# Kernel optimization log

Hardware: AMD Instinct MI355X
Metric: run time of the kernel (lower is better)

The kernel has to match this reference:

```python
import jax, jax.numpy as jnp
import numpy as np

N, E, B = 100000, 800000, 64
IN, HC1, HC2, NC, SA = 256, 128, 32, 2, 350
NEG = 0.2  # GATv2Conv default negative_slope


def forward(s_x, s_edge_index, s_batch, s_root_n_id,
            Wq, bq, Wk, bk, Wv, bv,
            Wl1, bl1, Wr1, br1, att1, bias1,
            Wl2, bl2, Wr2, br2, att2, bias2,
            Wl3, bl3, Wr3, br3, att3, bias3,
            c1w, c1b, c2W, c2b, c3W, c3b,
            linW, linb, aW1, ab1, aW2, mW1, mb1, mW2, mb2):
    src, dst = s_edge_index[0], s_edge_index[1]
    x_info = s_x
    # --- SelfAttention over seq_len=1 (x.unsqueeze(1)) ---
    z = s_x[:, None, :]                                   # [N,1,IN]
    q = z @ Wq + bq; k = z @ Wk + bk; v = z @ Wv + bv      # [N,1,SA]
    scores = jnp.einsum('nqd,nkd->nqk', q, k) / jnp.sqrt(jnp.float32(SA))
    probs = jax.nn.softmax(scores, axis=-1)
    h = jnp.einsum('nqk,nkd->nqd', probs, v)[:, 0, :]      # [N,SA]

    def gatv2(x, Wl, bl, Wr, br, att, bias):
        # PyG GATv2Conv, heads=1, eval mode (dropout off)
        xl = x @ Wl + bl                                   # source transform [N,O]
        xr = x @ Wr + br                                   # target transform [N,O]
        e = jax.nn.leaky_relu(xl[src] + xr[dst], NEG)      # [E,O]
        s = e @ att                                        # [E]
        smax = jax.ops.segment_max(s, dst, num_segments=N)
        smax = jnp.where(jnp.isfinite(smax), smax, 0.0)
        ex = jnp.exp(s - smax[dst])
        den = jax.ops.segment_sum(ex, dst, num_segments=N)
        alpha = ex / jnp.maximum(den[dst], 1e-16)
        return jax.ops.segment_sum(alpha[:, None] * xl[src], dst, num_segments=N) + bias

    h = jax.nn.relu(gatv2(h, Wl1, bl1, Wr1, br1, att1, bias1))
    h = jax.nn.relu(gatv2(h, Wl2, bl2, Wr2, br2, att2, bias2))
    h = jax.nn.relu(gatv2(h, Wl3, bl3, Wr3, br3, att3, bias3))   # [N,HC2]

    # --- readout: root node feature ++ global mean pool ---
    cnt = jax.ops.segment_sum(jnp.ones((N,), h.dtype), s_batch, num_segments=B)
    pooled = jax.ops.segment_sum(h, s_batch, num_segments=B) / jnp.maximum(cnt, 1.0)[:, None]
    sx = jnp.concatenate([h[s_root_n_id], pooled], axis=-1)       # [B,2*HC2]

    # --- info branch on raw root features ---
    info = x_info[s_root_n_id]                                    # [B,IN]
    info = c1w[0] * info[:, :-2] + c1w[1] * info[:, 1:-1] + c1w[2] * info[:, 2:] + c1b  # Conv1d(1,1,3)
    t = info.T                                                    # [IN-2,B]
    t = jax.nn.relu(c2W @ t + c2b[:, None])                       # [HC1,B]
    t = jax.nn.relu(c3W @ t + c3b[:, None])                       # [HC1//2,B]
    t = t.T                                                       # [B,HC1//2]
    L = t.shape[1]
    t = jax.nn.relu(t.reshape(B, HC2, L // HC2).mean(-1))         # AdaptiveAvgPool1d(HC2)

    sx = jax.nn.relu(sx @ linW + linb)                            # [B,HC2]

    # --- semantic attention over the two views ---
    emb = jnp.stack([sx, t], axis=1)                              # [B,2,HC2]
    w = jnp.tanh(emb @ aW1 + ab1) @ aW2                           # [B,2,1]
    beta = jax.nn.softmax(w, axis=1)
    emb = (beta * emb).sum(1)                                     # [B,HC2]

    return jax.nn.softmax(jnp.tanh(emb @ mW1 + mb1) @ mW2 + mb2, axis=1)  # [B,NC]


def setup_inputs() -> dict:
    keys = iter(jax.random.split(jax.random.key(0), 64))
    def nrm(*shape):
        return jax.random.normal(next(keys), shape, dtype=jnp.float32) * 0.05
    inp = {}
    inp['s_x'] = jax.random.normal(next(keys), (N, IN), dtype=jnp.float32)
    inp['s_edge_index'] = jax.random.randint(next(keys), (2, E), 0, N)
    inp['s_batch'] = jnp.sort(jax.random.randint(next(keys), (N,), 0, B))
    inp['s_root_n_id'] = jax.random.randint(next(keys), (B,), 0, N)
    inp['Wq'] = nrm(IN, SA); inp['bq'] = nrm(SA)
    inp['Wk'] = nrm(IN, SA); inp['bk'] = nrm(SA)
    inp['Wv'] = nrm(IN, SA); inp['bv'] = nrm(SA)
    inp['Wl1'] = nrm(SA, HC1); inp['bl1'] = nrm(HC1)
    inp['Wr1'] = nrm(SA, HC1); inp['br1'] = nrm(HC1)
    inp['att1'] = nrm(HC1); inp['bias1'] = nrm(HC1)
    inp['Wl2'] = nrm(HC1, HC1 // 2); inp['bl2'] = nrm(HC1 // 2)
    inp['Wr2'] = nrm(HC1, HC1 // 2); inp['br2'] = nrm(HC1 // 2)
    inp['att2'] = nrm(HC1 // 2); inp['bias2'] = nrm(HC1 // 2)
    inp['Wl3'] = nrm(HC1 // 2, HC2); inp['bl3'] = nrm(HC2)
    inp['Wr3'] = nrm(HC1 // 2, HC2); inp['br3'] = nrm(HC2)
    inp['att3'] = nrm(HC2); inp['bias3'] = nrm(HC2)
    inp['c1w'] = nrm(3); inp['c1b'] = nrm(1)
    inp['c2W'] = nrm(HC1, IN - 2); inp['c2b'] = nrm(HC1)
    inp['c3W'] = nrm(HC1 // 2, HC1); inp['c3b'] = nrm(HC1 // 2)
    inp['linW'] = nrm(2 * HC2, HC2); inp['linb'] = nrm(HC2)
    inp['aW1'] = nrm(HC2, 16); inp['ab1'] = nrm(16); inp['aW2'] = nrm(16, 1)
    inp['mW1'] = nrm(HC2, 16); inp['mb1'] = nrm(16)
    inp['mW2'] = nrm(16, NC); inp['mb2'] = nrm(NC)
    return inp


def reference(s_x, s_edge_index, s_batch, s_root_n_id,
              Wq, bq, Wk, bk, Wv, bv,
              Wl1, bl1, Wr1, br1, att1, bias1,
              Wl2, bl2, Wr2, br2, att2, bias2,
              Wl3, bl3, Wr3, br3, att3, bias3,
              c1w, c1b, c2W, c2b, c3W, c3b,
              linW, linb, aW1, ab1, aW2, mW1, mb1, mW2, mb2):
    return forward(s_x, s_edge_index, s_batch, s_root_n_id,
                   Wq, bq, Wk, bk, Wv, bv,
                   Wl1, bl1, Wr1, br1, att1, bias1,
                   Wl2, bl2, Wr2, br2, att2, bias2,
                   Wl3, bl3, Wr3, br3, att3, bias3,
                   c1w, c1b, c2W, c2b, c3W, c3b,
                   linW, linb, aW1, ab1, aW2, mW1, mb1, mW2, mb2)
```

## Files before the change

### kernel.cpp

```cpp
#include <hip/hip_runtime.h>
#include <hip/hip_bf16.h>
#include <math.h>

typedef unsigned short ushort_t;
typedef __attribute__((ext_vector_type(8))) short bfrag;
typedef __attribute__((ext_vector_type(4))) float ffrag;

constexpr int N_NODES = 100000;
constexpr int N_EDGES = 800000;
constexpr int NB      = 64;
constexpr int IN_F    = 256;
constexpr int HC1C    = 128;
constexpr int HC2C    = 32;
constexpr int SA_D    = 350;
constexpr float NEG   = 0.2f;

constexpr int SCAN_NBLK = (N_NODES + 255) / 256;
constexpr int MB128     = (N_NODES + 127) / 128;

constexpr size_t OFF_WT1    = 0;
constexpr size_t OFF_WT2    = OFF_WT1 + 65536;
constexpr size_t OFF_WT3    = OFF_WT2 + 16384;
constexpr size_t OFF_BC1    = OFF_WT3 + 4096;
constexpr size_t OFF_BC2    = OFF_BC1 + 256;
constexpr size_t OFF_BC3    = OFF_BC2 + 128;
constexpr size_t OFF_XLR    = OFF_BC3 + 64;
constexpr size_t OFF_H      = OFF_XLR + (size_t)N_NODES * 256;
constexpr size_t OFF_DEG    = OFF_H + (size_t)N_NODES * 128;
constexpr size_t OFF_ROWPTR = OFF_DEG + N_NODES;
constexpr size_t OFF_CURSOR = OFF_ROWPTR + N_NODES + 1;
constexpr size_t OFF_BLKS   = OFF_CURSOR + N_NODES;
constexpr size_t OFF_BLKO   = OFF_BLKS + 512;
constexpr size_t OFF_CSRSRC = OFF_BLKO + 512;
constexpr size_t OFF_POOLED = OFF_CSRSRC + N_EDGES;
constexpr size_t OFF_CNT    = OFF_POOLED + NB * HC2C;
constexpr size_t OFF_SX     = OFF_CNT + NB;
constexpr size_t OFF_INFO   = OFF_SX + NB * HC2C;
constexpr size_t OFF_T1     = OFF_INFO + (size_t)NB * (IN_F - 2);
constexpr size_t OFF_T2     = OFF_T1 + (size_t)HC1C * NB;
constexpr size_t OFF_TT     = OFF_T2 + (size_t)NB * NB;
constexpr size_t WS_FLOATS  = OFF_TT + NB * HC2C;

__device__ __forceinline__ ushort_t f2bf(float f) {
  union { float f; unsigned int u; } a;
  a.f = f;
  unsigned int r = a.u + 0x7FFFu + ((a.u >> 16) & 1u);
  return (ushort_t)(r >> 16);
}
__device__ __forceinline__ float bf2f(ushort_t h) {
  union { unsigned int u; float f; } a;
  a.u = ((unsigned int)h) << 16;
  return a.f;
}
__device__ __forceinline__ float2 bfp(unsigned int u) {
  float2 r;
  r.x = __uint_as_float(u << 16);
  r.y = __uint_as_float(u & 0xFFFF0000u);
  return r;
}
__device__ __forceinline__ unsigned int pack2(float a, float b) {
  unsigned int ua = __float_as_uint(a);
  ua += 0x7FFFu + ((ua >> 16) & 1u);
  unsigned int ub = __float_as_uint(b);
  ub += 0x7FFFu + ((ub >> 16) & 1u);
  return __builtin_amdgcn_perm(ub, ua, 0x07060302u);
}

__global__ void k_wcomb(const float* __restrict__ Wv, const float* __restrict__ Wl1,
                        const float* __restrict__ Wr1, ushort_t* __restrict__ WT) {
  int t = blockIdx.x * blockDim.x + threadIdx.x;
  if (t >= 256 * 256) return;
  int n = t & 255;
  int k = t >> 8;
  const float* Wx = (n < 128) ? Wl1 : Wr1;
  int j = n & 127;
  float a = 0.f;
  for (int kk = 0; kk < SA_D; ++kk) a += Wv[k * SA_D + kk] * Wx[kk * 128 + j];
  WT[(size_t)n * 256 + k] = f2bf(a);
}

__global__ void k_bcomb(const float* __restrict__ bv, const float* __restrict__ Wl1,
                        const float* __restrict__ bl1, const float* __restrict__ Wr1,
                        const float* __restrict__ br1, float* __restrict__ bc) {
  int n = threadIdx.x;
  if (n >= 256) return;
  const float* Wx = (n < 128) ? Wl1 : Wr1;
  const float* bx = (n < 128) ? bl1 : br1;
  int j = n & 127;
  float a = bx[j];
  for (int kk = 0; kk < SA_D; ++kk) a += bv[kk] * Wx[kk * 128 + j];
  bc[n] = a;
}

template <int K, int C>
__global__ void k_wpack(const float* __restrict__ Wl, const float* __restrict__ bl,
                        const float* __restrict__ Wr, const float* __restrict__ br,
                        ushort_t* __restrict__ WT, float* __restrict__ bc) {
  constexpr int NN = 2 * C;
  int t = blockIdx.x * blockDim.x + threadIdx.x;
  if (t < NN) bc[t] = (t < C) ? bl[t] : br[t - C];
  if (t >= NN * K) return;
  int n = t % NN;
  int k = t / NN;
  float v = (n < C) ? Wl[k * C + n] : Wr[k * C + (n - C)];
  WT[(size_t)n * K + k] = f2bf(v);
}

__global__ void k_hist(const int* __restrict__ dst, int* __restrict__ deg) {
  int e = blockIdx.x * blockDim.x + threadIdx.x;
  if (e < N_EDGES) atomicAdd(deg + dst[e], 1);
}

__global__ void k_scan_local(const int* __restrict__ deg, int* __restrict__ row_ptr,
                             int* __restrict__ blk_sum) {
  __shared__ int sh[256];
  int t = threadIdx.x;
  int i = blockIdx.x * 256 + t;
  int v = (i < N_NODES) ? deg[i] : 0;
  sh[t] = v;
  __syncthreads();
  for (int off = 1; off < 256; off <<= 1) {
    int add = (t >= off) ? sh[t - off] : 0;
    __syncthreads();
    sh[t] += add;
    __syncthreads();
  }
  if (i < N_NODES) row_ptr[i] = sh[t] - v;
  if (t == 255) blk_sum[blockIdx.x] = sh[255];
}

__global__ void k_scan_blk(const int* __restrict__ blk_sum, int* __restrict__ blk_off) {
  __shared__ int sh[512];
  int t = threadIdx.x;
  int v = (t < SCAN_NBLK) ? blk_sum[t] : 0;
  sh[t] = v;
  __syncthreads();
  for (int off = 1; off < 512; off <<= 1) {
    int add = (t >= off) ? sh[t - off] : 0;
    __syncthreads();
    sh[t] += add;
    __syncthreads();
  }
  blk_off[t] = sh[t] - v;
}

__global__ void k_scan_add(int* __restrict__ row_ptr, const int* __restrict__ blk_off,
                           int* __restrict__ cursor) {
  int i = blockIdx.x * blockDim.x + threadIdx.x;
  if (i < N_NODES) {
    int v = row_ptr[i] + blk_off[i >> 8];
    row_ptr[i] = v;
    cursor[i] = v;
  }
  if (i == 0) row_ptr[N_NODES] = N_EDGES;
}

__global__ void k_fill(const int* __restrict__ src, const int* __restrict__ dst,
                       int* __restrict__ cursor, int* __restrict__ csr_src) {
  int e = blockIdx.x * blockDim.x + threadIdx.x;
  if (e >= N_EDGES) return;
  int pos = atomicAdd(cursor + dst[e], 1);
  csr_src[pos] = src[e];
}

template <int K, int NN, int BN, bool AF32>
__global__ __launch_bounds__(256) void k_gemm_bf16(const void* __restrict__ xin,
                                                   const ushort_t* __restrict__ WT,
                                                   const float* __restrict__ bc,
                                                   ushort_t* __restrict__ out, int M) {
  constexpr int BM    = 128;
  constexpr int BK    = 32;
  constexpr int LDA   = BK + 8;
  constexpr int RT    = 4;
  constexpr int CT    = BN / 32;
  constexpr int NSTEP = K / BK;
  constexpr int NBCH  = (BN * 4) / 256;
  __shared__ ushort_t As[2][BM * LDA];
  __shared__ ushort_t Bs[2][BN * LDA];
  const int tid  = threadIdx.x;
  const int wave = tid >> 6;
  const int wrow = wave >> 1;
  const int wcol = wave & 1;
  const int lane = tid & 63;
  const int quad = lane >> 4;
  const int l16  = lane & 15;
  const int m0   = blockIdx.x * BM;
  const int n0   = blockIdx.y * BN;

  const int arow = tid >> 1;
  const int aks  = (tid & 1) * 16;
  int gm = m0 + arow;
  if (gm >= M) gm = M - 1;

  float4 fA[4];
  uint4  uA[2];
  uint4  uB[NBCH];

  auto loadT = [&](int k0) {
    if (AF32) {
      const float4* sp = (const float4*)((const float*)xin + (size_t)gm * K + k0 + aks);
      fA[0] = sp[0]; fA[1] = sp[1]; fA[2] = sp[2]; fA[3] = sp[3];
    } else {
      const uint4* sp = (const uint4*)((const ushort_t*)xin + (size_t)gm * K + k0 + aks);
      uA[0] = sp[0]; uA[1] = sp[1];
    }
#pragma unroll
    for (int c = 0; c < NBCH; ++c) {
      int ch = tid + c * 256;
      int n  = ch >> 2;
      int ks = (ch & 3) * 8;
      uB[c] = *(const uint4*)(WT + (size_t)(n0 + n) * K + k0 + ks);
    }
  };
  auto storeT = [&](int buf) {
    if (AF32) {
      uint4 p0, p1;
      p0.x = pack2(fA[0].x, fA[0].y); p0.y = pack2(fA[0].z, fA[0].w);
      p0.z = pack2(fA[1].x, fA[1].y); p0.w = pack2(fA[1].z, fA[1].w);
      p1.x = pack2(fA[2].x, fA[2].y); p1.y = pack2(fA[2].z, fA[2].w);
      p1.z = pack2(fA[3].x, fA[3].y); p1.w = pack2(fA[3].z, fA[3].w);
      *(uint4*)&As[buf][arow * LDA + aks]     = p0;
      *(uint4*)&As[buf][arow * LDA + aks + 8] = p1;
    } else {
      *(uint4*)&As[buf][arow * LDA + aks]     = uA[0];
      *(uint4*)&As[buf][arow * LDA + aks + 8] = uA[1];
    }
#pragma unroll
    for (int c = 0; c < NBCH; ++c) {
      int ch = tid + c * 256;
      int n  = ch >> 2;
      int ks = (ch & 3) * 8;
      *(uint4*)&Bs[buf][n * LDA + ks] = uB[c];
    }
  };

  ffrag acc[RT][CT];
#pragma unroll
  for (int rt = 0; rt < RT; ++rt)
#pragma unroll
    for (int ct = 0; ct < CT; ++ct) acc[rt][ct] = ffrag{0.f, 0.f, 0.f, 0.f};

  loadT(0);
  storeT(0);
  __syncthreads();

  for (int i = 0; i < NSTEP; ++i) {
    const int cur = i & 1;
    if (i + 1 < NSTEP) loadT((i + 1) * BK);
    bfrag a[RT], b[CT];
#pragma unroll
    for (int rt = 0; rt < RT; ++rt)
      a[rt] = *(const bfrag*)&As[cur][(wrow * 64 + rt * 16 + l16) * LDA + quad * 8];
#pragma unroll
    for (int ct = 0; ct < CT; ++ct)
      b[ct] = *(const bfrag*)&Bs[cur][(wcol * (BN / 2) + ct * 16 + l16) * LDA + quad * 8];
#pragma unroll
    for (int ct = 0; ct < CT; ++ct)
#pragma unroll
      for (int rt = 0; rt < RT; ++rt)
        acc[rt][ct] = __builtin_amdgcn_mfma_f32_16x16x32_bf16(a[rt], b[ct], acc[rt][ct], 0, 0, 0);
    if (i + 1 < NSTEP) storeT(1 - cur);
    __syncthreads();
  }

#pragma unroll
  for (int rt = 0; rt < RT; ++rt)
#pragma unroll
    for (int ct = 0; ct < CT; ++ct) {
      int n = n0 + wcol * (BN / 2) + ct * 16 + l16;
      float b = bc[n];
#pragma unroll
      for (int r = 0; r < 4; ++r) {
        int m = m0 + wrow * 64 + rt * 16 + quad * 4 + r;
        if (m < M) out[(size_t)m * NN + n] = f2bf(acc[rt][ct][r] + b);
      }
    }
}

template <int C>
__global__ void k_gat(const ushort_t* __restrict__ xlr, const int* __restrict__ row_ptr,
                      const int* __restrict__ csr_src, const float* __restrict__ att,
                      const float* __restrict__ bias, ushort_t* __restrict__ h) {
  constexpr int G = C / 8;
  constexpr int RS = 2 * C;
  int t = blockIdx.x * blockDim.x + threadIdx.x;
  int d = t / G;
  int lane = t - d * G;
  if (d >= N_NODES) return;
  float xr[8], a[8];
  {
    uint4 u = *(const uint4*)(xlr + (size_t)d * RS + C + lane * 8);
    float2 p0 = bfp(u.x), p1 = bfp(u.y), p2 = bfp(u.z), p3 = bfp(u.w);
    xr[0] = p0.x; xr[1] = p0.y; xr[2] = p1.x; xr[3] = p1.y;
    xr[4] = p2.x; xr[5] = p2.y; xr[6] = p3.x; xr[7] = p3.y;
  }
  *(float4*)&a[0] = *(const float4*)(att + lane * 8);
  *(float4*)&a[4] = *(const float4*)(att + lane * 8 + 4);
  float acc[8];
#pragma unroll
  for (int j = 0; j < 8; ++j) acc[j] = 0.f;
  float den = 0.f;
  const int e0 = row_ptr[d], e1 = row_ptr[d + 1];
  for (int i = e0; i < e1; ++i) {
    int s = csr_src[i];
    uint4 u = *(const uint4*)(xlr + (size_t)s * RS + lane * 8);
    float xl[8];
    {
      float2 p0 = bfp(u.x), p1 = bfp(u.y), p2 = bfp(u.z), p3 = bfp(u.w);
      xl[0] = p0.x; xl[1] = p0.y; xl[2] = p1.x; xl[3] = p1.y;
      xl[4] = p2.x; xl[5] = p2.y; xl[6] = p3.x; xl[7] = p3.y;
    }
    float p = 0.f;
#pragma unroll
    for (int j = 0; j < 8; ++j) {
      float v = xl[j] + xr[j];
      v = v > 0.f ? v : NEG * v;
      p += a[j] * v;
    }
#pragma unroll
    for (int off = G / 2; off > 0; off >>= 1) p += __shfl_xor(p, off, 64);
    float ex = expf(p);
    den += ex;
#pragma unroll
    for (int j = 0; j < 8; ++j) acc[j] += ex * xl[j];
  }
  float inv = 1.f / fmaxf(den, 1e-16f);
  float o[8];
#pragma unroll
  for (int j = 0; j < 8; ++j)
    o[j] = fmaxf(acc[j] * inv + bias[lane * 8 + j], 0.f);
  uint4 pk;
  pk.x = pack2(o[0], o[1]);
  pk.y = pack2(o[2], o[3]);
  pk.z = pack2(o[4], o[5]);
  pk.w = pack2(o[6], o[7]);
  *(uint4*)(h + (size_t)d * C + lane * 8) = pk;
}

__global__ void k_pool(const ushort_t* __restrict__ h3, const int* __restrict__ batch,
                       float* __restrict__ pooled, float* __restrict__ cnt) {
  constexpr int NPB = 1024;
  constexpr int NPT = NPB / 8;
  int c = threadIdx.x & 31;
  int r = threadIdx.x >> 5;
  int base = blockIdx.x * NPB + r * NPT;
  if (base >= N_NODES) return;
  int end = base + NPT;
  if (end > N_NODES) end = N_NODES;
  int cur_b = batch[base];
  float acc = 0.f, count = 0.f;
  for (int n = base; n < end; ++n) {
    int b = batch[n];
    if (b != cur_b) {
      atomicAdd(pooled + cur_b * HC2C + c, acc);
      if (c == 0) atomicAdd(cnt + cur_b, count);
      cur_b = b;
      acc = 0.f;
      count = 0.f;
    }
    acc += bf2f(h3[(size_t)n * HC2C + c]);
    count += 1.f;
  }
  atomicAdd(pooled + cur_b * HC2C + c, acc);
  if (c == 0) atomicAdd(cnt + cur_b, count);
}

__global__ void k_sx(const ushort_t* __restrict__ h3, const int* __restrict__ root,
                     const float* __restrict__ pooled, const float* __restrict__ cnt,
                     const float* __restrict__ linW, const float* __restrict__ linb,
                     float* __restrict__ sx) {
  int t = blockIdx.x * blockDim.x + threadIdx.x;
  if (t >= NB * HC2C) return;
  int b = t >> 5, j = t & 31;
  int r = root[b];
  float inv = 1.f / fmaxf(cnt[b], 1.0f);
  float a = linb[j];
  for (int c = 0; c < HC2C; ++c) a += bf2f(h3[(size_t)r * HC2C + c]) * linW[c * HC2C + j];
  for (int c = 0; c < HC2C; ++c) a += (pooled[b * HC2C + c] * inv) * linW[(HC2C + c) * HC2C + j];
  sx[t] = a > 0.f ? a : 0.f;
}

__global__ void k_info1(const float* __restrict__ X, const int* __restrict__ root,
                        const float* __restrict__ c1w, const float* __restrict__ c1b,
                        float* __restrict__ info) {
  constexpr int L = IN_F - 2;
  int t = blockIdx.x * blockDim.x + threadIdx.x;
  if (t >= NB * L) return;
  int b = t / L, i = t - (t / L) * L;
  const float* xr = X + (size_t)root[b] * IN_F;
  info[t] = c1w[0] * xr[i] + c1w[1] * xr[i + 1] + c1w[2] * xr[i + 2] + c1b[0];
}

__global__ void k_info2(const float* __restrict__ info, const float* __restrict__ c2W,
                        const float* __restrict__ c2b, float* __restrict__ t1) {
  constexpr int L = IN_F - 2;
  int t = blockIdx.x * blockDim.x + threadIdx.x;
  if (t >= HC1C * NB) return;
  int j = t >> 6, b = t & 63;
  float a = c2b[j];
  for (int i = 0; i < L; ++i) a += c2W[j * L + i] * info[b * L + i];
  t1[t] = a > 0.f ? a : 0.f;
}

__global__ void k_info3(const float* __restrict__ t1, const float* __restrict__ c3W,
                        const float* __restrict__ c3b, float* __restrict__ t2) {
  int t = blockIdx.x * blockDim.x + threadIdx.x;
  if (t >= NB * NB) return;
  int j = t >> 6, b = t & 63;
  float a = c3b[j];
  for (int i = 0; i < HC1C; ++i) a += c3W[j * HC1C + i] * t1[i * NB + b];
  t2[t] = a > 0.f ? a : 0.f;
}

__global__ void k_info4(const float* __restrict__ t2, float* __restrict__ tt) {
  int t = blockIdx.x * blockDim.x + threadIdx.x;
  if (t >= NB * HC2C) return;
  int b = t >> 5, c = t & 31;
  float v = 0.5f * (t2[(2 * c) * NB + b] + t2[(2 * c + 1) * NB + b]);
  tt[b * HC2C + c] = v > 0.f ? v : 0.f;
}

__global__ void k_final(const float* __restrict__ sx, const float* __restrict__ tt,
                        const float* __restrict__ aW1, const float* __restrict__ ab1,
                        const float* __restrict__ aW2, const float* __restrict__ mW1,
                        const float* __restrict__ mb1, const float* __restrict__ mW2,
                        const float* __restrict__ mb2, float* __restrict__ out) {
  int b = threadIdx.x;
  if (b >= NB) return;
  const float* e0 = sx + b * HC2C;
  const float* e1 = tt + b * HC2C;
  float w[2];
#pragma unroll
  for (int r = 0; r < 2; ++r) {
    const float* eb = (r == 0) ? e0 : e1;
    float acc = 0.f;
    for (int j = 0; j < 16; ++j) {
      float z = ab1[j];
      for (int c = 0; c < HC2C; ++c) z += eb[c] * aW1[c * 16 + j];
      acc += tanhf(z) * aW2[j];
    }
    w[r] = acc;
  }
  float mx = fmaxf(w[0], w[1]);
  float x0 = expf(w[0] - mx), x1 = expf(w[1] - mx);
  float inv = 1.f / (x0 + x1);
  float b0 = x0 * inv, b1 = x1 * inv;
  float t16[16];
  for (int j = 0; j < 16; ++j) {
    float z = mb1[j];
    for (int c = 0; c < HC2C; ++c) z += (b0 * e0[c] + b1 * e1[c]) * mW1[c * 16 + j];
    t16[j] = tanhf(z);
  }
  float l0 = mb2[0], l1 = mb2[1];
  for (int j = 0; j < 16; ++j) {
    l0 += t16[j] * mW2[j * 2 + 0];
    l1 += t16[j] * mW2[j * 2 + 1];
  }
  float m2 = fmaxf(l0, l1);
  float y0 = expf(l0 - m2), y1 = expf(l1 - m2);
  float is = 1.f / (y0 + y1);
  out[b * 2 + 0] = y0 * is;
  out[b * 2 + 1] = y1 * is;
}

extern "C" void kernel_launch(void* const* d_in, const int* in_sizes, int n_in, void* d_out,
                              int out_size, void* d_ws, size_t ws_size, hipStream_t stream) {
  if (ws_size < WS_FLOATS * sizeof(float)) return;

  const float* s_x   = (const float*)d_in[0];
  const int*   edge  = (const int*)d_in[1];
  const int*   batch = (const int*)d_in[2];
  const int*   root  = (const int*)d_in[3];
  const float* Wv    = (const float*)d_in[8];
  const float* bv    = (const float*)d_in[9];
  const float* Wl1   = (const float*)d_in[10];
  const float* bl1   = (const float*)d_in[11];
  const float* Wr1   = (const float*)d_in[12];
  const float* br1   = (const float*)d_in[13];
  const float* att1  = (const float*)d_in[14];
  const float* bias1 = (const float*)d_in[15];
  const float* Wl2   = (const float*)d_in[16];
  const float* bl2   = (const float*)d_in[17];
  const float* Wr2   = (const float*)d_in[18];
  const float* br2   = (const float*)d_in[19];
  const float* att2  = (const float*)d_in[20];
  const float* bias2 = (const float*)d_in[21];
  const float* Wl3   = (const float*)d_in[22];
  const float* bl3   = (const float*)d_in[23];
  const float* Wr3   = (const float*)d_in[24];
  const float* br3   = (const float*)d_in[25];
  const float* att3  = (const float*)d_in[26];
  const float* bias3 = (const float*)d_in[27];
  const float* c1w   = (const float*)d_in[28];
  const float* c1b   = (const float*)d_in[29];
  const float* c2W   = (const float*)d_in[30];
  const float* c2b   = (const float*)d_in[31];
  const float* c3W   = (const float*)d_in[32];
  const float* c3b   = (const float*)d_in[33];
  const float* linW  = (const float*)d_in[34];
  const float* linb  = (const float*)d_in[35];
  const float* aW1   = (const float*)d_in[36];
  const float* ab1   = (const float*)d_in[37];
  const float* aW2   = (const float*)d_in[38];
  const float* mW1   = (const float*)d_in[39];
  const float* mb1   = (const float*)d_in[40];
  const float* mW2   = (const float*)d_in[41];
  const float* mb2   = (const float*)d_in[42];

  const int* src = edge;
  const int* dst = edge + N_EDGES;

  float*    ws      = (float*)d_ws;
  ushort_t* WT1     = (ushort_t*)(ws + OFF_WT1);
  ushort_t* WT2     = (ushort_t*)(ws + OFF_WT2);
  ushort_t* WT3     = (ushort_t*)(ws + OFF_WT3);
  float*    bc1     = ws + OFF_BC1;
  float*    bc2     = ws + OFF_BC2;
  float*    bc3     = ws + OFF_BC3;
  ushort_t* xlr     = (ushort_t*)(ws + OFF_XLR);
  ushort_t* hbuf    = (ushort_t*)(ws + OFF_H);
  int*      deg     = (int*)(ws + OFF_DEG);
  int*      row_ptr = (int*)(ws + OFF_ROWPTR);
  int*      cursor  = (int*)(ws + OFF_CURSOR);
  int*      blks    = (int*)(ws + OFF_BLKS);
  int*      blko    = (int*)(ws + OFF_BLKO);
  int*      csr_src = (int*)(ws + OFF_CSRSRC);
  float*    pooled  = ws + OFF_POOLED;
  float*    cnt     = ws + OFF_CNT;
  float*    sx      = ws + OFF_SX;
  float*    info    = ws + OFF_INFO;
  float*    t1      = ws + OFF_T1;
  float*    t2      = ws + OFF_T2;
  float*    tt      = ws + OFF_TT;
  float*    out     = (float*)d_out;

  hipMemsetAsync(deg, 0, N_NODES * sizeof(int), stream);
  k_hist<<<(N_EDGES + 255) / 256, 256, 0, stream>>>(dst, deg);
  k_scan_local<<<SCAN_NBLK, 256, 0, stream>>>(deg, row_ptr, blks);
  k_scan_blk<<<1, 512, 0, stream>>>(blks, blko);
  k_scan_add<<<SCAN_NBLK, 256, 0, stream>>>(row_ptr, blko, cursor);
  k_fill<<<(N_EDGES + 255) / 256, 256, 0, stream>>>(src, dst, cursor, csr_src);

  k_wcomb<<<(256 * 256) / 256, 256, 0, stream>>>(Wv, Wl1, Wr1, WT1);
  k_bcomb<<<1, 256, 0, stream>>>(bv, Wl1, bl1, Wr1, br1, bc1);
  k_wpack<128, 64><<<(128 * 128 + 255) / 256, 256, 0, stream>>>(Wl2, bl2, Wr2, br2, WT2, bc2);
  k_wpack<64, 32><<<(64 * 64 + 255) / 256, 256, 0, stream>>>(Wl3, bl3, Wr3, br3, WT3, bc3);

  k_gemm_bf16<256, 256, 128, true><<<dim3(MB128, 2), 256, 0, stream>>>(s_x, WT1, bc1, xlr,
                                                                       N_NODES);
  k_gat<128><<<(N_NODES * 16 + 255) / 256, 256, 0, stream>>>(xlr, row_ptr, csr_src, att1,
                                                             bias1, hbuf);

  k_gemm_bf16<128, 128, 128, false><<<dim3(MB128, 1), 256, 0, stream>>>(hbuf, WT2, bc2, xlr,
                                                                        N_NODES);
  k_gat<64><<<(N_NODES * 8 + 255) / 256, 256, 0, stream>>>(xlr, row_ptr, csr_src, att2,
                                                           bias2, hbuf);

  k_gemm_bf16<64, 64, 64, false><<<dim3(MB128, 1), 256, 0, stream>>>(hbuf, WT3, bc3, xlr,
                                                                     N_NODES);
  k_gat<32><<<(N_NODES * 4 + 255) / 256, 256, 0, stream>>>(xlr, row_ptr, csr_src, att3,
                                                           bias3, hbuf);

  hipMemsetAsync(pooled, 0, (NB * HC2C + NB) * sizeof(float), stream);
  k_pool<<<(N_NODES + 1023) / 1024, 256, 0, stream>>>(hbuf, batch, pooled, cnt);
  k_sx<<<(NB * HC2C + 255) / 256, 256, 0, stream>>>(hbuf, root, pooled, cnt, linW, linb, sx);

  k_info1<<<(NB * (IN_F - 2) + 255) / 256, 256, 0, stream>>>(s_x, root, c1w, c1b, info);
  k_info2<<<(HC1C * NB + 255) / 256, 256, 0, stream>>>(info, c2W, c2b, t1);
  k_info3<<<(NB * NB + 255) / 256, 256, 0, stream>>>(t1, c3W, c3b, t2);
  k_info4<<<(NB * HC2C + 255) / 256, 256, 0, stream>>>(t2, tt);

  k_final<<<1, NB, 0, stream>>>(sx, tt, aW1, ab1, aW2, mW1, mb1, mW2, mb2, out);
}
```

Before: 680.8 us.

## Widen GEMM K-tile to 64 single-buffered and unroll GAT edge loop by two

The bf16 MFMA GEMM goes from a double-buffered BK=32 register-prefetch pipeline to a single-buffered BK=64 tile, doing two MFMA k-halves per barrier. This halves the number of K steps and synchronisations but gives up the overlap of global loads with compute. Separately, the GAT aggregation loop now handles two edges per iteration, with independent gathers and shuffle reductions, to expose more memory-level parallelism on the irregular source-row loads. The GAT unroll adds register pressure and a tail case for odd-degree nodes.

```diff
diff --git a/kernel.cpp b/kernel.cpp
--- a/kernel.cpp
+++ b/kernel.cpp
@@ -169,14 +169,13 @@
                                                    const float* __restrict__ bc,
                                                    ushort_t* __restrict__ out, int M) {
   constexpr int BM    = 128;
-  constexpr int BK    = 32;
+  constexpr int BK    = 64;
   constexpr int LDA   = BK + 8;
   constexpr int RT    = 4;
   constexpr int CT    = BN / 32;
   constexpr int NSTEP = K / BK;
-  constexpr int NBCH  = (BN * 4) / 256;
-  __shared__ ushort_t As[2][BM * LDA];
-  __shared__ ushort_t Bs[2][BN * LDA];
+  __shared__ ushort_t As[BM * LDA];
+  __shared__ ushort_t Bs[BN * LDA];
   const int tid  = threadIdx.x;
   const int wave = tid >> 6;
   const int wrow = wave >> 1;
@@ -188,79 +187,65 @@
   const int n0   = blockIdx.y * BN;
 
   const int arow = tid >> 1;
-  const int aks  = (tid & 1) * 16;
+  const int aks  = (tid & 1) * 32;
   int gm = m0 + arow;
   if (gm >= M) gm = M - 1;
 
-  float4 fA[4];
-  uint4  uA[2];
-  uint4  uB[NBCH];
-
-  auto loadT = [&](int k0) {
+  ffrag acc[RT][CT];
+#pragma unroll
+  for (int rt = 0; rt < RT; ++rt)
+#pragma unroll
+    for (int ct = 0; ct < CT; ++ct) acc[rt][ct] = ffrag{0.f, 0.f, 0.f, 0.f};
+
+  for (int i = 0; i < NSTEP; ++i) {
+    const int k0 = i * BK;
+    if (i) __syncthreads();
     if (AF32) {
       const float4* sp = (const float4*)((const float*)xin + (size_t)gm * K + k0 + aks);
-      fA[0] = sp[0]; fA[1] = sp[1]; fA[2] = sp[2]; fA[3] = sp[3];
+      float4 f[8];
+#pragma unroll
+      for (int j = 0; j < 8; ++j) f[j] = sp[j];
+      unsigned int d[16];
+#pragma unroll
+      for (int j = 0; j < 8; ++j) {
+        d[2 * j]     = pack2(f[j].x, f[j].y);
+        d[2 * j + 1] = pack2(f[j].z, f[j].w);
+      }
+#pragma unroll
+      for (int j = 0; j < 4; ++j)
+        *(uint4*)&As[arow * LDA + aks + j * 8] = *(uint4*)&d[j * 4];
     } else {
       const uint4* sp = (const uint4*)((const ushort_t*)xin + (size_t)gm * K + k0 + aks);
-      uA[0] = sp[0]; uA[1] = sp[1];
-    }
-#pragma unroll
-    for (int c = 0; c < NBCH; ++c) {
+      uint4 u[4];
+#pragma unroll
+      for (int j = 0; j < 4; ++j) u[j] = sp[j];
+#pragma unroll
+      for (int j = 0; j < 4; ++j)
+        *(uint4*)&As[arow * LDA + aks + j * 8] = u[j];
+    }
+#pragma unroll
+    for (int c = 0; c < BN / 32; ++c) {
       int ch = tid + c * 256;
-      int n  = ch >> 2;
-      int ks = (ch & 3) * 8;
-      uB[c] = *(const uint4*)(WT + (size_t)(n0 + n) * K + k0 + ks);
-    }
-  };
-  auto storeT = [&](int buf) {
-    if (AF32) {
-      uint4 p0, p1;
-      p0.x = pack2(fA[0].x, fA[0].y); p0.y = pack2(fA[0].z, fA[0].w);
-      p0.z = pack2(fA[1].x, fA[1].y); p0.w = pack2(fA[1].z, fA[1].w);
-      p1.x = pack2(fA[2].x, fA[2].y); p1.y = pack2(fA[2].z, fA[2].w);
-      p1.z = pack2(fA[3].x, fA[3].y); p1.w = pack2(fA[3].z, fA[3].w);
-      *(uint4*)&As[buf][arow * LDA + aks]     = p0;
-      *(uint4*)&As[buf][arow * LDA + aks + 8] = p1;
-    } else {
-      *(uint4*)&As[buf][arow * LDA + aks]     = uA[0];
-      *(uint4*)&As[buf][arow * LDA + aks + 8] = uA[1];
-    }
-#pragma unroll
-    for (int c = 0; c < NBCH; ++c) {
-      int ch = tid + c * 256;
-      int n  = ch >> 2;
-      int ks = (ch & 3) * 8;
-      *(uint4*)&Bs[buf][n * LDA + ks] = uB[c];
-    }
-  };
-
-  ffrag acc[RT][CT];
-#pragma unroll
-  for (int rt = 0; rt < RT; ++rt)
-#pragma unroll
-    for (int ct = 0; ct < CT; ++ct) acc[rt][ct] = ffrag{0.f, 0.f, 0.f, 0.f};
-
-  loadT(0);
-  storeT(0);
-  __syncthreads();
-
-  for (int i = 0; i < NSTEP; ++i) {
-    const int cur = i & 1;
-    if (i + 1 < NSTEP) loadT((i + 1) * BK);
-    bfrag a[RT], b[CT];
-#pragma unroll
-    for (int rt = 0; rt < RT; ++rt)
-      a[rt] = *(const bfrag*)&As[cur][(wrow * 64 + rt * 16 + l16) * LDA + quad * 8];
-#pragma unroll
-    for (int ct = 0; ct < CT; ++ct)
-      b[ct] = *(const bfrag*)&Bs[cur][(wcol * (BN / 2) + ct * 16 + l16) * LDA + quad * 8];
-#pragma unroll
-    for (int ct = 0; ct < CT; ++ct)
+      int n  = ch >> 3;
+      int ks = (ch & 7) * 8;
+      *(uint4*)&Bs[n * LDA + ks] = *(const uint4*)(WT + (size_t)(n0 + n) * K + k0 + ks);
+    }
+    __syncthreads();
+#pragma unroll
+    for (int kh = 0; kh < 2; ++kh) {
+      bfrag a[RT], b[CT];
 #pragma unroll
       for (int rt = 0; rt < RT; ++rt)
-        acc[rt][ct] = __builtin_amdgcn_mfma_f32_16x16x32_bf16(a[rt], b[ct], acc[rt][ct], 0, 0, 0);
-    if (i + 1 < NSTEP) storeT(1 - cur);
-    __syncthreads();
+        a[rt] = *(const bfrag*)&As[(wrow * 64 + rt * 16 + l16) * LDA + kh * 32 + quad * 8];
+#pragma unroll
+      for (int ct = 0; ct < CT; ++ct)
+        b[ct] = *(const bfrag*)&Bs[(wcol * (BN / 2) + ct * 16 + l16) * LDA + kh * 32 + quad * 8];
+#pragma unroll
+      for (int ct = 0; ct < CT; ++ct)
+#pragma unroll
+        for (int rt = 0; rt < RT; ++rt)
+          acc[rt][ct] = __builtin_amdgcn_mfma_f32_16x16x32_bf16(a[rt], b[ct], acc[rt][ct], 0, 0, 0);
+    }
   }
 
 #pragma unroll
@@ -301,14 +286,50 @@
   for (int j = 0; j < 8; ++j) acc[j] = 0.f;
   float den = 0.f;
   const int e0 = row_ptr[d], e1 = row_ptr[d + 1];
-  for (int i = e0; i < e1; ++i) {
+  int i = e0;
+  for (; i + 2 <= e1; i += 2) {
+    int s0 = csr_src[i];
+    int s1 = csr_src[i + 1];
+    uint4 u0 = *(const uint4*)(xlr + (size_t)s0 * RS + lane * 8);
+    uint4 u1 = *(const uint4*)(xlr + (size_t)s1 * RS + lane * 8);
+    float xl0[8], xl1[8];
+    {
+      float2 q0 = bfp(u0.x), q1 = bfp(u0.y), q2 = bfp(u0.z), q3 = bfp(u0.w);
+      xl0[0] = q0.x; xl0[1] = q0.y; xl0[2] = q1.x; xl0[3] = q1.y;
+      xl0[4] = q2.x; xl0[5] = q2.y; xl0[6] = q3.x; xl0[7] = q3.y;
+      float2 r0 = bfp(u1.x), r1 = bfp(u1.y), r2 = bfp(u1.z), r3 = bfp(u1.w);
+      xl1[0] = r0.x; xl1[1] = r0.y; xl1[2] = r1.x; xl1[3] = r1.y;
+      xl1[4] = r2.x; xl1[5] = r2.y; xl1[6] = r3.x; xl1[7] = r3.y;
+    }
+    float p0 = 0.f, p1 = 0.f;
+#pragma unroll
+    for (int j = 0; j < 8; ++j) {
+      float v0 = xl0[j] + xr[j];
+      v0 = v0 > 0.f ? v0 : NEG * v0;
+      p0 += a[j] * v0;
+      float v1 = xl1[j] + xr[j];
+      v1 = v1 > 0.f ? v1 : NEG * v1;
+      p1 += a[j] * v1;
+    }
+#pragma unroll
+    for (int off = G / 2; off > 0; off >>= 1) {
+      p0 += __shfl_xor(p0, off, 64);
+      p1 += __shfl_xor(p1, off, 64);
+    }
+    float ex0 = expf(p0);
+    float ex1 = expf(p1);
+    den += ex0 + ex1;
+#pragma unroll
+    for (int j = 0; j < 8; ++j) acc[j] += ex0 * xl0[j] + ex1 * xl1[j];
+  }
+  if (i < e1) {
     int s = csr_src[i];
     uint4 u = *(const uint4*)(xlr + (size_t)s * RS + lane * 8);
     float xl[8];
     {
-      float2 p0 = bfp(u.x), p1 = bfp(u.y), p2 = bfp(u.z), p3 = bfp(u.w);
-      xl[0] = p0.x; xl[1] = p0.y; xl[2] = p1.x; xl[3] = p1.y;
-      xl[4] = p2.x; xl[5] = p2.y; xl[6] = p3.x; xl[7] = p3.y;
+      float2 q0 = bfp(u.x), q1 = bfp(u.y), q2 = bfp(u.z), q3 = bfp(u.w);
+      xl[0] = q0.x; xl[1] = q0.y; xl[2] = q1.x; xl[3] = q1.y;
+      xl[4] = q2.x; xl[5] = q2.y; xl[6] = q3.x; xl[7] = q3.y;
     }
     float p = 0.f;
 #pragma unroll
```

Result: faster. 655.1 us (-3.8%).
